# Kernel optimization log

Measured on AMD Instinct MI355X. Metric: run time of the kernel, lower is better.

Reference implementation:

```python
import jax, jax.numpy as jnp
import numpy as np

DIM = 512
NSLOTS = 8
ITERS = 3
EPS = 1e-8
LN_EPS = 1e-5
SCALE = DIM ** -0.5


def _ln(x, g, b):
    m = jnp.mean(x, axis=-1, keepdims=True)
    v = jnp.mean((x - m) ** 2, axis=-1, keepdims=True)
    return (x - m) / jnp.sqrt(v + LN_EPS) * g + b


def _gru(x, h, W_ih, W_hh, b_ih, b_hh):
    # PyTorch GRUCell, gate order r,z,n
    gi = x @ W_ih.T + b_ih
    gh = h @ W_hh.T + b_hh
    ir, iz, inn = jnp.split(gi, 3, axis=-1)
    hr, hz, hn = jnp.split(gh, 3, axis=-1)
    r = jax.nn.sigmoid(ir + hr)
    z = jax.nn.sigmoid(iz + hz)
    n = jnp.tanh(inn + r * hn)
    return (1.0 - z) * n + z * h


def _norm_attn(dots):
    # softmax over slot axis, then renormalize over token axis
    a = jax.nn.softmax(dots, axis=1)
    return a / (jnp.sum(a, axis=-1, keepdims=True) + EPS)


def setup_inputs() -> dict:
    key = jax.random.key(0)
    ks = jax.random.split(key, 16)
    b, na, ni = 32, 1024, 3136
    d, hd = DIM, DIM  # hidden_dim = max(dim, 128) = 512
    s = 0.02
    inp = {
        'inputs_audio': jax.random.normal(ks[0], (b, na, d), jnp.float32),
        'inputs_image': jax.random.normal(ks[1], (b, ni, d), jnp.float32),
        'slots_noise': jax.random.normal(ks[2], (b, NSLOTS, d), jnp.float32),
        'slots_mu': jax.random.normal(ks[3], (1, 1, d), jnp.float32),
        'slots_logsigma': jnp.zeros((1, 1, d), jnp.float32),
        'ln_in_g': jnp.ones((d,), jnp.float32), 'ln_in_b': jnp.zeros((d,), jnp.float32),
        'ln_slots_g': jnp.ones((d,), jnp.float32), 'ln_slots_b': jnp.zeros((d,), jnp.float32),
        'ln_ff_g': jnp.ones((d,), jnp.float32), 'ln_ff_b': jnp.zeros((d,), jnp.float32),
        'Wq': jax.random.normal(ks[4], (d, d), jnp.float32) * s, 'bq': jnp.zeros((d,), jnp.float32),
        'Wk': jax.random.normal(ks[5], (d, d), jnp.float32) * s, 'bk': jnp.zeros((d,), jnp.float32),
        'Wv': jax.random.normal(ks[6], (d, d), jnp.float32) * s, 'bv': jnp.zeros((d,), jnp.float32),
        'W_ih': jax.random.normal(ks[7], (3 * d, d), jnp.float32) * s,
        'W_hh': jax.random.normal(ks[8], (3 * d, d), jnp.float32) * s,
        'b_ih': jnp.zeros((3 * d,), jnp.float32), 'b_hh': jnp.zeros((3 * d,), jnp.float32),
        'W1': jax.random.normal(ks[9], (hd, d), jnp.float32) * s, 'b1': jnp.zeros((hd,), jnp.float32),
        'W2': jax.random.normal(ks[10], (d, hd), jnp.float32) * s, 'b2': jnp.zeros((d,), jnp.float32),
    }
    return inp


def reference(inputs_audio, inputs_image, slots_noise, slots_mu, slots_logsigma,
              ln_in_g, ln_in_b, ln_slots_g, ln_slots_b, ln_ff_g, ln_ff_b,
              Wq, bq, Wk, bk, Wv, bv, W_ih, W_hh, b_ih, b_hh, W1, b1, W2, b2):
    b, na, d = inputs_audio.shape
    slots0 = slots_mu + jnp.exp(slots_logsigma) * slots_noise  # [b, S, d]

    ia = _ln(inputs_audio, ln_in_g, ln_in_b)
    ii = _ln(inputs_image, ln_in_g, ln_in_b)
    k_a = ia @ Wk.T + bk
    v_a = ia @ Wv.T + bv
    k_i = ii @ Wk.T + bk
    v_i = ii @ Wv.T + bv

    def mlp(x):
        return jax.nn.relu(x @ W1.T + b1) @ W2.T + b2

    def step(slots, k, v):
        prev = slots
        sn = _ln(slots, ln_slots_g, ln_slots_b)
        q = sn @ Wq.T + bq
        dots = jnp.einsum('bid,bjd->bij', q, k) * SCALE
        attn = _norm_attn(dots)
        upd = jnp.einsum('bjd,bij->bid', v, attn)
        h = _gru(upd.reshape(-1, d), prev.reshape(-1, d), W_ih, W_hh, b_ih, b_hh)
        slots = h.reshape(b, -1, d)
        slots = slots + mlp(_ln(slots, ln_ff_g, ln_ff_b))
        return slots, q, attn

    slots_a, slots_i = slots0, slots0
    for _ in range(ITERS):
        slots_a, q_a, attn_a = step(slots_a, k_a, v_a)
        slots_i, q_i, attn_i = step(slots_i, k_i, v_i)

    cross_ai = _norm_attn(jnp.einsum('bid,bjd->bij', q_a, k_i) * SCALE)  # audio->image
    cross_ia = _norm_attn(jnp.einsum('bid,bjd->bij', q_i, k_a) * SCALE)  # image->audio

    return (slots_a, q_a, k_a, attn_a, cross_ia,
            slots_i, q_i, k_i, attn_i, cross_ai)
```

## Files before the change

kernel.cpp:

```cpp
#include <hip/hip_runtime.h>
#include <hip/hip_bf16.h>

#define DIM 512
#define EPS 1e-8f
#define LN_EPS 1e-5f
#define SCALE 0.04419417382415922f

typedef float f32x4 __attribute__((ext_vector_type(4)));
typedef __bf16 bf16;
typedef __bf16 bf16x8 __attribute__((ext_vector_type(8)));

typedef const __attribute__((address_space(1))) void gvoid;
typedef __attribute__((address_space(3))) void lvoid;

__device__ inline float bf2f_lo(unsigned u) { union { unsigned x; float f; } c; c.x = u << 16; return c.f; }
__device__ inline float bf2f_hi(unsigned u) { union { unsigned x; float f; } c; c.x = u & 0xffff0000u; return c.f; }

__global__ __launch_bounds__(256) void k_stats_convert(
    const float* __restrict__ x, bf16* __restrict__ xbf,
    float* __restrict__ stats, int M)
{
  int row = blockIdx.x * 4 + (threadIdx.x >> 6);
  int lane = threadIdx.x & 63;
  if (row >= M) return;
  const float* xr = x + (size_t)row * DIM;
  float4 a = *(const float4*)(xr + lane * 8);
  float4 b = *(const float4*)(xr + lane * 8 + 4);
  float s  = a.x + a.y + a.z + a.w + b.x + b.y + b.z + b.w;
  float ss = a.x*a.x + a.y*a.y + a.z*a.z + a.w*a.w
           + b.x*b.x + b.y*b.y + b.z*b.z + b.w*b.w;
  for (int off = 32; off; off >>= 1) { s += __shfl_xor(s, off); ss += __shfl_xor(ss, off); }
  float mean = s * (1.0f / DIM);
  float var  = ss * (1.0f / DIM) - mean * mean;
  float rs   = rsqrtf(var + LN_EPS);
  if (lane == 0) { stats[row * 2] = mean; stats[row * 2 + 1] = rs; }
  union { bf16 h[8]; uint4 u; } cv;
  cv.h[0] = (bf16)a.x; cv.h[1] = (bf16)a.y; cv.h[2] = (bf16)a.z; cv.h[3] = (bf16)a.w;
  cv.h[4] = (bf16)b.x; cv.h[5] = (bf16)b.y; cv.h[6] = (bf16)b.z; cv.h[7] = (bf16)b.w;
  *(uint4*)(xbf + (size_t)row * DIM + lane * 8) = cv.u;
}

__global__ __launch_bounds__(256) void k_stats512(
    const float* __restrict__ x, float* __restrict__ stats)
{
  int row = blockIdx.x * 4 + (threadIdx.x >> 6);
  int lane = threadIdx.x & 63;
  const float* xr = x + (size_t)row * DIM;
  float4 a = *(const float4*)(xr + lane * 8);
  float4 b = *(const float4*)(xr + lane * 8 + 4);
  float s  = a.x + a.y + a.z + a.w + b.x + b.y + b.z + b.w;
  float ss = a.x*a.x + a.y*a.y + a.z*a.z + a.w*a.w
           + b.x*b.x + b.y*b.y + b.z*b.z + b.w*b.w;
  for (int off = 32; off; off >>= 1) { s += __shfl_xor(s, off); ss += __shfl_xor(ss, off); }
  float mean = s * (1.0f / DIM);
  float rs   = rsqrtf(ss * (1.0f / DIM) - mean * mean + LN_EPS);
  if (lane == 0) { stats[row * 2] = mean; stats[row * 2 + 1] = rs; }
}

__global__ __launch_bounds__(64) void k_prep(
    const float* __restrict__ Wk, const float* __restrict__ bk,
    const float* __restrict__ Wv, const float* __restrict__ bv,
    const float* __restrict__ g_in, const float* __restrict__ b_in,
    const float* __restrict__ Wq, const float* __restrict__ bq,
    const float* __restrict__ g_s, const float* __restrict__ b_s,
    const float* __restrict__ W1, const float* __restrict__ b1,
    const float* __restrict__ g_f, const float* __restrict__ b_f,
    bf16* __restrict__ wbf, float* __restrict__ c12kv,
    float* __restrict__ Wqp, float* __restrict__ cq,
    float* __restrict__ W1p, float* __restrict__ c1f)
{
  int n = blockIdx.x; int lane = threadIdx.x;
  if (n < 1024) {
    const float* W = (n < DIM) ? (Wk + (size_t)n * DIM) : (Wv + (size_t)(n - DIM) * DIM);
    float bias = (n < DIM) ? bk[n] : bv[n - DIM];
    float s1 = 0.f, s2 = 0.f;
    union { bf16 h[8]; uint4 u; } cv;
#pragma unroll
    for (int j = 0; j < 8; ++j) {
      int d = lane * 8 + j;
      float w = W[d];
      float gw = g_in[d] * w;
      s1 += gw; s2 += b_in[d] * w;
      cv.h[j] = (bf16)gw;
    }
    *(uint4*)(wbf + (size_t)n * DIM + lane * 8) = cv.u;
    for (int off = 32; off; off >>= 1) { s1 += __shfl_xor(s1, off); s2 += __shfl_xor(s2, off); }
    if (lane == 0) { c12kv[n * 2] = s1; c12kv[n * 2 + 1] = s2 + bias; }
  } else {
    int m; const float* W; float bias; const float* g; const float* b;
    float* Wp; float* cc;
    if (n < 1536) { m = n - 1024; W = Wq + (size_t)m * DIM; bias = bq[m]; g = g_s; b = b_s; Wp = Wqp; cc = cq; }
    else          { m = n - 1536; W = W1 + (size_t)m * DIM; bias = b1[m]; g = g_f; b = b_f; Wp = W1p; cc = c1f; }
    float s1 = 0.f, s2 = 0.f;
    float arr[8];
#pragma unroll
    for (int j = 0; j < 8; ++j) {
      int d = lane * 8 + j;
      float w = W[d];
      float gw = g[d] * w;
      s1 += gw; s2 += b[d] * w;
      arr[j] = gw;
    }
    *(float4*)(Wp + (size_t)m * DIM + lane * 8)     = make_float4(arr[0], arr[1], arr[2], arr[3]);
    *(float4*)(Wp + (size_t)m * DIM + lane * 8 + 4) = make_float4(arr[4], arr[5], arr[6], arr[7]);
    for (int off = 32; off; off >>= 1) { s1 += __shfl_xor(s1, off); s2 += __shfl_xor(s2, off); }
    if (lane == 0) { cc[m * 2] = s1; cc[m * 2 + 1] = s2 + bias; }
  }
}

__global__ __launch_bounds__(256) void k_kv_gemm(
    const bf16* __restrict__ xbf, const bf16* __restrict__ wbf,
    const float* __restrict__ stats, const float* __restrict__ c12,
    float* __restrict__ kout, bf16* __restrict__ kbf, bf16* __restrict__ vbf,
    int nblk)
{
  __shared__ bf16 As[2][128 * 64];
  __shared__ bf16 Bs[2][128 * 64];
  const int t = threadIdx.x, wave = t >> 6, lane = t & 63;
  int bid = blockIdx.x;
  int rid = (bid & 7) * (nblk >> 3) + (bid >> 3);
  const int row0 = (rid >> 3) * 128, col0 = (rid & 7) * 128;
  f32x4 acc[4][4] = {};

  const int sr  = wave * 8 + (lane >> 3);
  const int sgl = ((lane & 7) ^ (lane >> 3)) * 8;
  const bf16* asrc = xbf + (size_t)(row0 + sr) * DIM + sgl;
  const bf16* bsrc = wbf + (size_t)(col0 + sr) * DIM + sgl;

  auto stage = [&](int buf, int k0) {
#pragma unroll
    for (int p = 0; p < 4; ++p) {
      __builtin_amdgcn_global_load_lds(
          (gvoid*)(asrc + (size_t)p * 32 * DIM + k0),
          (lvoid*)((char*)&As[buf][0] + (p * 256 + wave * 64) * 16), 16, 0, 0);
      __builtin_amdgcn_global_load_lds(
          (gvoid*)(bsrc + (size_t)p * 32 * DIM + k0),
          (lvoid*)((char*)&Bs[buf][0] + (p * 256 + wave * 64) * 16), 16, 0, 0);
    }
  };

  stage(0, 0);
  const int l15 = lane & 15, q16 = lane >> 4;
  const int wm = wave >> 1, wn = wave & 1;
  int cur = 0;
  for (int ks = 0; ks < 8; ++ks) {
    __syncthreads();
    if (ks < 7) stage(cur ^ 1, (ks + 1) * 64);
    const bf16* Ab = &As[cur][0];
    const bf16* Bb = &Bs[cur][0];
#pragma unroll
    for (int kk = 0; kk < 2; ++kk) {
      bf16x8 af[4], bfr[4];
#pragma unroll
      for (int mi = 0; mi < 4; ++mi) {
        int R = wm * 64 + mi * 16 + l15;
        int gp = (kk * 4 + q16) ^ (R & 7);
        af[mi] = *(const bf16x8*)(Ab + R * 64 + gp * 8);
      }
#pragma unroll
      for (int ni = 0; ni < 4; ++ni) {
        int R = wn * 64 + ni * 16 + l15;
        int gp = (kk * 4 + q16) ^ (R & 7);
        bfr[ni] = *(const bf16x8*)(Bb + R * 64 + gp * 8);
      }
#pragma unroll
      for (int mi = 0; mi < 4; ++mi)
#pragma unroll
        for (int ni = 0; ni < 4; ++ni)
          acc[mi][ni] = __builtin_amdgcn_mfma_f32_16x16x32_bf16(af[mi], bfr[ni], acc[mi][ni], 0, 0, 0);
    }
    cur ^= 1;
  }
  const int rbase = q16 * 4;
#pragma unroll
  for (int mi = 0; mi < 4; ++mi) {
#pragma unroll
    for (int reg = 0; reg < 4; ++reg) {
      int row = row0 + wm * 64 + mi * 16 + rbase + reg;
      float mean = stats[row * 2], rs = stats[row * 2 + 1];
#pragma unroll
      for (int ni = 0; ni < 4; ++ni) {
        int col = col0 + wn * 64 + ni * 16 + l15;
        float c1 = c12[col * 2], c2 = c12[col * 2 + 1];
        float outv = rs * acc[mi][ni][reg] - rs * mean * c1 + c2;
        if (col0 < DIM) {
          kout[(size_t)row * DIM + col] = outv;
          if (kbf) kbf[(size_t)row * DIM + col] = (bf16)outv;
        } else {
          vbf[(size_t)row * DIM + (col - DIM)] = (bf16)outv;
        }
      }
    }
  }
}

__global__ __launch_bounds__(256) void k_f2bf(
    const float* __restrict__ in, bf16* __restrict__ out)
{
  size_t i = ((size_t)blockIdx.x * 256 + threadIdx.x) * 8;
  float4 a = *(const float4*)(in + i);
  float4 b = *(const float4*)(in + i + 4);
  union { bf16 h[8]; uint4 u; } cv;
  cv.h[0] = (bf16)a.x; cv.h[1] = (bf16)a.y; cv.h[2] = (bf16)a.z; cv.h[3] = (bf16)a.w;
  cv.h[4] = (bf16)b.x; cv.h[5] = (bf16)b.y; cv.h[6] = (bf16)b.z; cv.h[7] = (bf16)b.w;
  *(uint4*)(out + i) = cv.u;
}

__global__ __launch_bounds__(256) void k_init_slots(
    const float* __restrict__ noise, const float* __restrict__ mu,
    const float* __restrict__ lsig, float* __restrict__ slots)
{
  int idx = blockIdx.x * 256 + threadIdx.x;
  int d = idx & (DIM - 1);
  float v = mu[d] + expf(lsig[d]) * noise[idx];
  slots[idx] = v;
  slots[131072 + idx] = v;
}

template <int MODE>
__global__ __launch_bounds__(128) void k_sgemm(
    const float* __restrict__ A, const float* __restrict__ B, int N,
    float* __restrict__ C,
    const float* __restrict__ c12, const float* __restrict__ stats,
    const float* __restrict__ bias, const float* __restrict__ invden,
    const float* __restrict__ R,
    float* __restrict__ outA, float* __restrict__ outI,
    bf16* __restrict__ qbf)
{
  __shared__ float As[32][33];
  __shared__ float Bs[64][33];
  int t = threadIdx.x;
  int m0 = blockIdx.y * 32, n0 = blockIdx.x * 64;
  float acc[4][4] = {};
  for (int k0 = 0; k0 < DIM; k0 += 32) {
    __syncthreads();
#pragma unroll
    for (int p = 0; p < 2; ++p) {
      int idx = p * 128 + t, r = idx >> 3, c4 = (idx & 7) * 4;
      float4 v = *(const float4*)(A + (size_t)(m0 + r) * DIM + k0 + c4);
      As[r][c4] = v.x; As[r][c4 + 1] = v.y; As[r][c4 + 2] = v.z; As[r][c4 + 3] = v.w;
    }
#pragma unroll
    for (int p = 0; p < 4; ++p) {
      int idx = p * 128 + t, r = idx >> 3, c4 = (idx & 7) * 4;
      float4 v = *(const float4*)(B + (size_t)(n0 + r) * DIM + k0 + c4);
      Bs[r][c4] = v.x; Bs[r][c4 + 1] = v.y; Bs[r][c4 + 2] = v.z; Bs[r][c4 + 3] = v.w;
    }
    __syncthreads();
    int tr = t >> 4, tc = t & 15;
#pragma unroll
    for (int k = 0; k < 32; ++k) {
      float a0 = As[tr * 4][k], a1 = As[tr * 4 + 1][k], a2 = As[tr * 4 + 2][k], a3 = As[tr * 4 + 3][k];
      float b0 = Bs[tc * 4][k], b1 = Bs[tc * 4 + 1][k], b2 = Bs[tc * 4 + 2][k], b3 = Bs[tc * 4 + 3][k];
      acc[0][0] += a0 * b0; acc[0][1] += a0 * b1; acc[0][2] += a0 * b2; acc[0][3] += a0 * b3;
      acc[1][0] += a1 * b0; acc[1][1] += a1 * b1; acc[1][2] += a1 * b2; acc[1][3] += a1 * b3;
      acc[2][0] += a2 * b0; acc[2][1] += a2 * b1; acc[2][2] += a2 * b2; acc[2][3] += a2 * b3;
      acc[3][0] += a3 * b0; acc[3][1] += a3 * b1; acc[3][2] += a3 * b2; acc[3][3] += a3 * b3;
    }
  }
  int tr = t >> 4, tc = t & 15;
#pragma unroll
  for (int mi = 0; mi < 4; ++mi) {
    int row = m0 + tr * 4 + mi;
#pragma unroll
    for (int ni = 0; ni < 4; ++ni) {
      int col = n0 + tc * 4 + ni;
      float v = acc[mi][ni];
      if (MODE == 0 || MODE == 3) {
        float mean = stats[row * 2], rs = stats[row * 2 + 1];
        v = rs * v - rs * mean * c12[col * 2] + c12[col * 2 + 1];
      }
      if (MODE == 1) v = v * invden[row] + bias[col];
      if (MODE == 2 || MODE == 4) v += bias[col];
      if (MODE == 3) v = fmaxf(v, 0.0f);
      if (MODE == 4) v += R[(size_t)row * N + col];
      if (MODE == 0) {
        if (row < 256) outA[(size_t)row * DIM + col] = v;
        else           outI[(size_t)(row - 256) * DIM + col] = v;
        qbf[(size_t)row * DIM + col] = (bf16)(v * SCALE);
      } else {
        C[(size_t)row * N + col] = v;
        if (MODE == 4 && outA) {
          if (row < 256) outA[(size_t)row * DIM + col] = v;
          else           outI[(size_t)(row - 256) * DIM + col] = v;
        }
      }
    }
  }
}

__global__ __launch_bounds__(256) void k_dots(
    const bf16* __restrict__ qA, const bf16* __restrict__ qI,
    const bf16* __restrict__ kA, const bf16* __restrict__ kI,
    float* __restrict__ aoutA, float* __restrict__ aoutI,
    float* __restrict__ denp, int NA_, int NI_)
{
  __shared__ bf16 ks[128 * 64];
  __shared__ float dsh[32];
  int t = threadIdx.x, wave = t >> 6, lane = t & 63;
  int b = blockIdx.y, tile = blockIdx.x;
  bool isA = tile < 8;
  int til = isA ? tile : tile - 8;
  int N = isA ? NA_ : NI_;
  int j0 = til * 128;
  const bf16* q = (isA ? qA : qI) + (size_t)b * 8 * DIM;
  const bf16* k = (isA ? kA : kI) + (size_t)b * N * DIM;
  float* aout = (isA ? aoutA : aoutI) + (size_t)b * 8 * N;
  int drow = (isA ? 0 : 256) + b * 8;

  const int l15 = lane & 15, q16 = lane >> 4;
  bf16x8 afq[16];
  {
    const bf16* qr = q + (size_t)(l15 & 7) * DIM + q16 * 8;
#pragma unroll
    for (int f = 0; f < 16; ++f)
      afq[f] = *(const bf16x8*)(qr + f * 32);
  }

  const int sr  = wave * 8 + (lane >> 3);
  const int sgl = ((lane & 7) ^ (lane >> 3)) * 8;
  f32x4 acc[2] = {};
  for (int c = 0; c < 8; ++c) {
    __syncthreads();
#pragma unroll
    for (int p = 0; p < 4; ++p) {
      int jr = j0 + p * 32 + sr;
      if (jr > N - 1) jr = N - 1;
      __builtin_amdgcn_global_load_lds(
          (gvoid*)(k + (size_t)jr * DIM + c * 64 + sgl),
          (lvoid*)((char*)ks + (p * 256 + wave * 64) * 16), 16, 0, 0);
    }
    __syncthreads();
#pragma unroll
    for (int kk = 0; kk < 2; ++kk) {
#pragma unroll
      for (int n = 0; n < 2; ++n) {
        int R = wave * 32 + n * 16 + l15;
        int gp = (kk * 4 + q16) ^ (R & 7);
        bf16x8 bfr = *(const bf16x8*)(ks + R * 64 + gp * 8);
        acc[n] = __builtin_amdgcn_mfma_f32_16x16x32_bf16(afq[c * 2 + kk], bfr, acc[n], 0, 0, 0);
      }
    }
  }

  float dsum[8];
#pragma unroll
  for (int i = 0; i < 8; ++i) dsum[i] = 0.f;
#pragma unroll
  for (int n = 0; n < 2; ++n) {
    int j = j0 + wave * 32 + n * 16 + l15;
    float dv[8];
#pragma unroll
    for (int r = 0; r < 4; ++r) {
      float own = acc[n][r];
      float oth = __shfl_xor(own, 16);
      if (q16 == 0) { dv[r] = own; dv[4 + r] = oth; }
      else          { dv[r] = oth; dv[4 + r] = own; }
    }
    float mx = dv[0];
#pragma unroll
    for (int i = 1; i < 8; ++i) mx = fmaxf(mx, dv[i]);
    float sum = 0.f;
#pragma unroll
    for (int i = 0; i < 8; ++i) { dv[i] = __expf(dv[i] - mx); sum += dv[i]; }
    float inv = 1.0f / sum;
    bool valid = (j < N);
#pragma unroll
    for (int i = 0; i < 8; ++i) {
      float av = valid ? dv[i] * inv : 0.0f;
      dsum[i] += av;
      if (valid && q16 == 0) aout[(size_t)i * N + j] = av;
    }
  }
#pragma unroll
  for (int i = 0; i < 8; ++i) {
    float v = dsum[i];
    v += __shfl_xor(v, 1); v += __shfl_xor(v, 2);
    v += __shfl_xor(v, 4); v += __shfl_xor(v, 8);
    dsum[i] = v;
  }
  if (lane == 0) {
#pragma unroll
    for (int i = 0; i < 8; ++i) dsh[wave * 8 + i] = dsum[i];
  }
  __syncthreads();
  if (t < 8) {
    float den = dsh[t] + dsh[8 + t] + dsh[16 + t] + dsh[24 + t];
    denp[((size_t)drow + t) * 32 + til] = den;
  }
}

__global__ __launch_bounds__(256) void k_upd(
    const bf16* __restrict__ vA, const bf16* __restrict__ vI,
    const float* __restrict__ aA, const float* __restrict__ aI,
    float* __restrict__ numpA, float* __restrict__ numpI, int NA_, int NI_)
{
  __shared__ float ash[128 * 12];
  int t = threadIdx.x, b = blockIdx.y, x = blockIdx.x;
  bool isA = x < 4;
  int c = isA ? x : x - 4;
  int N = isA ? NA_ : NI_;
  int nc = isA ? 4 : 13;
  int jstart = c * 256;
  int jend = jstart + 256; if (jend > N) jend = N;
  const bf16* v = (isA ? vA : vI) + (size_t)b * N * DIM;
  const float* a = (isA ? aA : aI) + (size_t)b * 8 * N;
  float acc[16] = {};
  int d0 = t * 2;
  for (int jt = jstart; jt < jend; jt += 128) {
    int jmax = jend - jt; if (jmax > 128) jmax = 128;
    __syncthreads();
    {
      int i = t >> 5, jq = (t & 31) * 4;
      float4 av = make_float4(0.f, 0.f, 0.f, 0.f);
      if (jt + jq < N) av = *(const float4*)&a[(size_t)i * N + jt + jq];
      ash[(jq + 0) * 12 + i] = av.x;
      ash[(jq + 1) * 12 + i] = av.y;
      ash[(jq + 2) * 12 + i] = av.z;
      ash[(jq + 3) * 12 + i] = av.w;
    }
    __syncthreads();
    for (int jj = 0; jj < jmax; ++jj) {
      unsigned vv = *(const unsigned*)(v + (size_t)(jt + jj) * DIM + d0);
      float v0 = bf2f_lo(vv), v1 = bf2f_hi(vv);
      float4 a0 = *(const float4*)&ash[jj * 12];
      float4 a1 = *(const float4*)&ash[jj * 12 + 4];
      acc[0]  += a0.x * v0; acc[1]  += a0.x * v1;
      acc[2]  += a0.y * v0; acc[3]  += a0.y * v1;
      acc[4]  += a0.z * v0; acc[5]  += a0.z * v1;
      acc[6]  += a0.w * v0; acc[7]  += a0.w * v1;
      acc[8]  += a1.x * v0; acc[9]  += a1.x * v1;
      acc[10] += a1.y * v0; acc[11] += a1.y * v1;
      acc[12] += a1.z * v0; acc[13] += a1.z * v1;
      acc[14] += a1.w * v0; acc[15] += a1.w * v1;
    }
  }
  float* np = (isA ? numpA : numpI) + (((size_t)b * nc + c) * 8) * DIM;
#pragma unroll
  for (int i = 0; i < 8; ++i)
    *(float2*)&np[(size_t)i * DIM + d0] = make_float2(acc[i * 2], acc[i * 2 + 1]);
}

__global__ __launch_bounds__(256) void k_numred(
    const float* __restrict__ numpA, const float* __restrict__ numpI,
    const float* __restrict__ denp,
    float* __restrict__ num, float* __restrict__ invden)
{
  int m = blockIdx.x, t = threadIdx.x;
  bool isA = m < 256;
  int mm = isA ? m : m - 256;
  int bb = mm >> 3, i = mm & 7;
  int nc = isA ? 4 : 13;
  const float* np = (isA ? numpA : numpI) + (((size_t)bb * nc) * 8 + i) * DIM;
  int d0 = t * 2;
  float s0 = 0.f, s1 = 0.f;
  for (int c = 0; c < nc; ++c) {
    float2 vv = *(const float2*)&np[(size_t)c * 8 * DIM + d0];
    s0 += vv.x; s1 += vv.y;
  }
  *(float2*)&num[(size_t)m * DIM + d0] = make_float2(s0, s1);
  if (t == 0) {
    int nch = isA ? 8 : 25;
    float den = EPS;
    for (int c2 = 0; c2 < nch; ++c2) den += denp[(size_t)m * 32 + c2];
    invden[m] = 1.0f / den;
  }
}

__global__ __launch_bounds__(256) void k_gru(
    const float* __restrict__ gi, const float* __restrict__ gh,
    const float* __restrict__ prev,
    float* __restrict__ hout, float* __restrict__ stats_h)
{
  int m = blockIdx.x; int t = threadIdx.x;
  size_t b3 = (size_t)m * 1536, b1 = (size_t)m * DIM;
  float h[2]; float s = 0.f, ss = 0.f;
#pragma unroll
  for (int p = 0; p < 2; ++p) {
    int d = t + p * 256;
    float ir = gi[b3 + d], iz = gi[b3 + 512 + d], in_ = gi[b3 + 1024 + d];
    float hr = gh[b3 + d], hz = gh[b3 + 512 + d], hn = gh[b3 + 1024 + d];
    float r = 1.f / (1.f + __expf(-(ir + hr)));
    float z = 1.f / (1.f + __expf(-(iz + hz)));
    float n = tanhf(in_ + r * hn);
    float hv = (1.f - z) * n + z * prev[b1 + d];
    hout[b1 + d] = hv;
    h[p] = hv; s += hv; ss += hv * hv;
  }
  for (int off = 32; off; off >>= 1) { s += __shfl_xor(s, off); ss += __shfl_xor(ss, off); }
  __shared__ float red[8];
  int wv = t >> 6, ln = t & 63;
  if (ln == 0) { red[wv] = s; red[4 + wv] = ss; }
  __syncthreads();
  s = red[0] + red[1] + red[2] + red[3];
  ss = red[4] + red[5] + red[6] + red[7];
  float mean = s * (1.0f / DIM);
  float rs = rsqrtf(ss * (1.0f / DIM) - mean * mean + LN_EPS);
  if (t == 0) { stats_h[m * 2] = mean; stats_h[m * 2 + 1] = rs; }
}

__global__ __launch_bounds__(256) void k_renorm2(
    const float* __restrict__ aA, const float* __restrict__ aI,
    const float* __restrict__ denp,
    float* __restrict__ outA, float* __restrict__ outI, int NA_, int NI_)
{
  int m = blockIdx.x; int t = threadIdx.x;
  bool isA = m < 256;
  int mm = isA ? m : m - 256;
  int N = isA ? NA_ : NI_;
  int nch = isA ? 8 : 25;
  const float* in = (isA ? aA : aI) + (size_t)mm * N;
  float* out = (isA ? outA : outI) + (size_t)mm * N;
  float den = EPS;
  for (int c = 0; c < nch; ++c) den += denp[(size_t)m * 32 + c];
  float inv = 1.0f / den;
  for (int idx = t; idx * 4 < N; idx += 256) {
    float4 v = *(const float4*)&in[idx * 4];
    v.x *= inv; v.y *= inv; v.z *= inv; v.w *= inv;
    *(float4*)&out[idx * 4] = v;
  }
}

extern "C" void kernel_launch(void* const* d_in, const int* in_sizes, int n_in,
                              void* d_out, int out_size, void* d_ws, size_t ws_size,
                              hipStream_t stream)
{
  (void)in_sizes; (void)n_in; (void)out_size;
  const float* x_a   = (const float*)d_in[0];
  const float* x_i   = (const float*)d_in[1];
  const float* noise = (const float*)d_in[2];
  const float* mu    = (const float*)d_in[3];
  const float* lsig  = (const float*)d_in[4];
  const float* ln_in_g = (const float*)d_in[5];
  const float* ln_in_b = (const float*)d_in[6];
  const float* ln_s_g  = (const float*)d_in[7];
  const float* ln_s_b  = (const float*)d_in[8];
  const float* ln_f_g  = (const float*)d_in[9];
  const float* ln_f_b  = (const float*)d_in[10];
  const float* Wq = (const float*)d_in[11]; const float* bq = (const float*)d_in[12];
  const float* Wk = (const float*)d_in[13]; const float* bk = (const float*)d_in[14];
  const float* Wv = (const float*)d_in[15]; const float* bv = (const float*)d_in[16];
  const float* W_ih = (const float*)d_in[17]; const float* W_hh = (const float*)d_in[18];
  const float* b_ih = (const float*)d_in[19]; const float* b_hh = (const float*)d_in[20];
  const float* W1 = (const float*)d_in[21]; const float* b1 = (const float*)d_in[22];
  const float* W2 = (const float*)d_in[23]; const float* b2 = (const float*)d_in[24];

  const int NA = 1024, NI = 3136;
  const int MA = 32 * NA, MI = 32 * NI;

  float* out = (float*)d_out;
  float* o_slots_a  = out;
  float* o_q_a      = out + 131072;
  float* o_k_a      = out + 262144;
  float* o_attn_a   = out + 17039360;
  float* o_cross_ia = out + 17301504;
  float* o_slots_i  = out + 17563648;
  float* o_q_i      = out + 17694720;
  float* o_k_i      = out + 17825792;
  float* o_attn_i   = out + 69206016;
  float* o_cross_ai = out + 70008832;

  char* w = (char*)d_ws;
  size_t used = 0;
  auto alloc = [&](size_t bytes) {
    char* p = w + used;
    used += (bytes + 255) & ~(size_t)255;
    return p;
  };
  bf16* xbf_a = (bf16*)alloc((size_t)MA * DIM * 2);
  bf16* xbf_i = (bf16*)alloc((size_t)MI * DIM * 2);
  bf16* vbf_a = (bf16*)alloc((size_t)MA * DIM * 2);
  bf16* vbf_i = (bf16*)alloc((size_t)MI * DIM * 2);
  float* stats_a = (float*)alloc((size_t)MA * 2 * 4);
  float* stats_i = (float*)alloc((size_t)MI * 2 * 4);
  bf16* wbf  = (bf16*)alloc(1024 * 512 * 2);
  float* c12kv = (float*)alloc(1024 * 2 * 4);
  float* Wqp = (float*)alloc(512 * 512 * 4);
  float* cq  = (float*)alloc(512 * 2 * 4);
  float* W1p = (float*)alloc(512 * 512 * 4);
  float* c1f = (float*)alloc(512 * 2 * 4);
  float* slots = (float*)alloc(512 * 512 * 4);
  bf16*  qbf   = (bf16*)alloc(512 * 512 * 2);
  float* mid   = (float*)alloc(512 * 512 * 4);
  float* hid   = (float*)alloc(512 * 512 * 4);
  float* num   = (float*)alloc(512 * 512 * 4);
  float* gib   = (float*)alloc(512 * 1536 * 4);
  float* ghb   = (float*)alloc(512 * 1536 * 4);
  float* stats_s = (float*)alloc(512 * 2 * 4);
  float* stats_h = (float*)alloc(512 * 2 * 4);
  float* invden  = (float*)alloc(512 * 4);
  float* denp    = (float*)alloc(512 * 32 * 4);
  float* abuf_a  = (float*)alloc((size_t)256 * NA * 4);
  float* abuf_i  = (float*)alloc((size_t)256 * NI * 4);
  float* numpA   = (float*)alloc((size_t)32 * 4 * 8 * DIM * 4);
  float* numpI   = (float*)alloc((size_t)32 * 13 * 8 * DIM * 4);
  if (used > ws_size) return;

  size_t kbf_bytes = (((size_t)MA * DIM * 2 + 255) & ~(size_t)255)
                   + (((size_t)MI * DIM * 2 + 255) & ~(size_t)255);
  bf16* kbf_a; bf16* kbf_i; bool kbf_fused;
  if (used + kbf_bytes <= ws_size) {
    kbf_a = (bf16*)alloc((size_t)MA * DIM * 2);
    kbf_i = (bf16*)alloc((size_t)MI * DIM * 2);
    kbf_fused = true;
  } else {
    kbf_a = xbf_a; kbf_i = xbf_i;
    kbf_fused = false;
  }

  k_stats_convert<<<MA / 4, 256, 0, stream>>>(x_a, xbf_a, stats_a, MA);
  k_stats_convert<<<MI / 4, 256, 0, stream>>>(x_i, xbf_i, stats_i, MI);
  k_prep<<<2048, 64, 0, stream>>>(Wk, bk, Wv, bv, ln_in_g, ln_in_b,
                                  Wq, bq, ln_s_g, ln_s_b, W1, b1, ln_f_g, ln_f_b,
                                  wbf, c12kv, Wqp, cq, W1p, c1f);
  k_kv_gemm<<<(MA / 128) * 8, 256, 0, stream>>>(xbf_a, wbf, stats_a, c12kv,
      o_k_a, kbf_fused ? kbf_a : nullptr, vbf_a, (MA / 128) * 8);
  k_kv_gemm<<<(MI / 128) * 8, 256, 0, stream>>>(xbf_i, wbf, stats_i, c12kv,
      o_k_i, kbf_fused ? kbf_i : nullptr, vbf_i, (MI / 128) * 8);
  if (!kbf_fused) {
    k_f2bf<<<MA * DIM / 2048, 256, 0, stream>>>(o_k_a, kbf_a);
    k_f2bf<<<MI * DIM / 2048, 256, 0, stream>>>(o_k_i, kbf_i);
  }
  k_init_slots<<<512, 256, 0, stream>>>(noise, mu, lsig, slots);
  k_stats512<<<128, 256, 0, stream>>>(slots, stats_s);

  for (int it = 0; it < 3; ++it) {
    bool last = (it == 2);
    k_sgemm<0><<<dim3(8, 16), 128, 0, stream>>>(slots, Wqp, DIM, nullptr,
        cq, stats_s, nullptr, nullptr, nullptr, o_q_a, o_q_i, qbf);
    k_dots<<<dim3(33, 32), 256, 0, stream>>>(qbf, qbf + 256 * DIM,
        kbf_a, kbf_i, abuf_a, abuf_i, denp, NA, NI);
    k_upd<<<dim3(17, 32), 256, 0, stream>>>(vbf_a, vbf_i, abuf_a, abuf_i, numpA, numpI, NA, NI);
    k_numred<<<512, 256, 0, stream>>>(numpA, numpI, denp, num, invden);
    k_sgemm<1><<<dim3(24, 16), 128, 0, stream>>>(num, W_ih, 1536, gib,
        nullptr, nullptr, b_ih, invden, nullptr, nullptr, nullptr, nullptr);
    k_sgemm<2><<<dim3(24, 16), 128, 0, stream>>>(slots, W_hh, 1536, ghb,
        nullptr, nullptr, b_hh, nullptr, nullptr, nullptr, nullptr, nullptr);
    k_gru<<<512, 256, 0, stream>>>(gib, ghb, slots, mid, stats_h);
    k_sgemm<3><<<dim3(8, 16), 128, 0, stream>>>(mid, W1p, DIM, hid,
        c1f, stats_h, nullptr, nullptr, nullptr, nullptr, nullptr, nullptr);
    k_sgemm<4><<<dim3(8, 16), 128, 0, stream>>>(hid, W2, DIM, slots,
        nullptr, nullptr, b2, nullptr, mid,
        last ? o_slots_a : nullptr, last ? o_slots_i : nullptr, nullptr);
    if (!last) k_stats512<<<128, 256, 0, stream>>>(slots, stats_s);
  }

  k_renorm2<<<512, 256, 0, stream>>>(abuf_a, abuf_i, denp, o_attn_a, o_attn_i, NA, NI);

  k_dots<<<dim3(33, 32), 256, 0, stream>>>(qbf + 256 * DIM, qbf,
      kbf_a, kbf_i, abuf_a, abuf_i, denp, NA, NI);
  k_renorm2<<<512, 256, 0, stream>>>(abuf_a, abuf_i, denp, o_cross_ia, o_cross_ai, NA, NI);
}
```

Baseline: 1.306 ms.

## Merge audio/image KV GEMMs into one launch with K=32 stages and vectorized epilogue

Combines the two K/V projection GEMM launches into a single grid that picks the audio or image operand per block. The K-step shrinks from 64 to 32, halving LDS use, and launch bounds request 4 blocks per CU to raise occupancy. MFMA operands are swapped so each lane holds four consecutive columns, letting the epilogue write float4 and packed bf16x4 stores. LN correction constants are split into separate c1/c2 arrays so they load as vectors. The cost is twice as many K-loop iterations and barriers per tile.

Measured after the change: 1.217 ms. 1.07x faster.

```diff
diff --git a/kernel.cpp b/kernel.cpp
--- a/kernel.cpp
+++ b/kernel.cpp
@@ -65,9 +65,9 @@
     const float* __restrict__ g_s, const float* __restrict__ b_s,
     const float* __restrict__ W1, const float* __restrict__ b1,
     const float* __restrict__ g_f, const float* __restrict__ b_f,
-    bf16* __restrict__ wbf, float* __restrict__ c12kv,
-    float* __restrict__ Wqp, float* __restrict__ cq,
-    float* __restrict__ W1p, float* __restrict__ c1f)
+    bf16* __restrict__ wbf, float* __restrict__ c1kv, float* __restrict__ c2kv,
+    float* __restrict__ Wqp, float* __restrict__ cq1, float* __restrict__ cq2,
+    float* __restrict__ W1p, float* __restrict__ cf1, float* __restrict__ cf2)
 {
   int n = blockIdx.x; int lane = threadIdx.x;
   if (n < 1024) {
@@ -85,12 +85,12 @@
     }
     *(uint4*)(wbf + (size_t)n * DIM + lane * 8) = cv.u;
     for (int off = 32; off; off >>= 1) { s1 += __shfl_xor(s1, off); s2 += __shfl_xor(s2, off); }
-    if (lane == 0) { c12kv[n * 2] = s1; c12kv[n * 2 + 1] = s2 + bias; }
+    if (lane == 0) { c1kv[n] = s1; c2kv[n] = s2 + bias; }
   } else {
     int m; const float* W; float bias; const float* g; const float* b;
-    float* Wp; float* cc;
-    if (n < 1536) { m = n - 1024; W = Wq + (size_t)m * DIM; bias = bq[m]; g = g_s; b = b_s; Wp = Wqp; cc = cq; }
-    else          { m = n - 1536; W = W1 + (size_t)m * DIM; bias = b1[m]; g = g_f; b = b_f; Wp = W1p; cc = c1f; }
+    float* Wp; float* cc1; float* cc2;
+    if (n < 1536) { m = n - 1024; W = Wq + (size_t)m * DIM; bias = bq[m]; g = g_s; b = b_s; Wp = Wqp; cc1 = cq1; cc2 = cq2; }
+    else          { m = n - 1536; W = W1 + (size_t)m * DIM; bias = b1[m]; g = g_f; b = b_f; Wp = W1p; cc1 = cf1; cc2 = cf2; }
     float s1 = 0.f, s2 = 0.f;
     float arr[8];
 #pragma unroll
@@ -104,91 +104,101 @@
     *(float4*)(Wp + (size_t)m * DIM + lane * 8)     = make_float4(arr[0], arr[1], arr[2], arr[3]);
     *(float4*)(Wp + (size_t)m * DIM + lane * 8 + 4) = make_float4(arr[4], arr[5], arr[6], arr[7]);
     for (int off = 32; off; off >>= 1) { s1 += __shfl_xor(s1, off); s2 += __shfl_xor(s2, off); }
-    if (lane == 0) { cc[m * 2] = s1; cc[m * 2 + 1] = s2 + bias; }
-  }
-}
-
-__global__ __launch_bounds__(256) void k_kv_gemm(
-    const bf16* __restrict__ xbf, const bf16* __restrict__ wbf,
-    const float* __restrict__ stats, const float* __restrict__ c12,
-    float* __restrict__ kout, bf16* __restrict__ kbf, bf16* __restrict__ vbf,
-    int nblk)
-{
-  __shared__ bf16 As[2][128 * 64];
-  __shared__ bf16 Bs[2][128 * 64];
+    if (lane == 0) { cc1[m] = s1; cc2[m] = s2 + bias; }
+  }
+}
+
+__global__ __launch_bounds__(256, 4) void k_kv_gemm(
+    const bf16* __restrict__ xa, const bf16* __restrict__ xi,
+    const bf16* __restrict__ wbf,
+    const float* __restrict__ sa, const float* __restrict__ si,
+    const float* __restrict__ c1, const float* __restrict__ c2,
+    float* __restrict__ ka, float* __restrict__ ki,
+    bf16* __restrict__ kba, bf16* __restrict__ kbi,
+    bf16* __restrict__ va, bf16* __restrict__ vi,
+    int nblkA, int nblkTot)
+{
+  __shared__ bf16 As[2][128 * 32];
+  __shared__ bf16 Bs[2][128 * 32];
   const int t = threadIdx.x, wave = t >> 6, lane = t & 63;
   int bid = blockIdx.x;
-  int rid = (bid & 7) * (nblk >> 3) + (bid >> 3);
-  const int row0 = (rid >> 3) * 128, col0 = (rid & 7) * 128;
+  int rid = (bid & 7) * (nblkTot >> 3) + (bid >> 3);
+  bool isA = rid < nblkA;
+  int lrid = isA ? rid : rid - nblkA;
+  const bf16* x = isA ? xa : xi;
+  const float* stats = isA ? sa : si;
+  float* kout = isA ? ka : ki;
+  bf16* kbf = isA ? kba : kbi;
+  bf16* vbf = isA ? va : vi;
+  const int row0 = (lrid >> 3) * 128, col0 = (lrid & 7) * 128;
   f32x4 acc[4][4] = {};
 
-  const int sr  = wave * 8 + (lane >> 3);
-  const int sgl = ((lane & 7) ^ (lane >> 3)) * 8;
-  const bf16* asrc = xbf + (size_t)(row0 + sr) * DIM + sgl;
+  const int sr  = wave * 16 + (lane >> 2);
+  const int sgl = ((lane & 3) ^ ((lane >> 3) & 3)) * 8;
+  const bf16* asrc = x   + (size_t)(row0 + sr) * DIM + sgl;
   const bf16* bsrc = wbf + (size_t)(col0 + sr) * DIM + sgl;
 
   auto stage = [&](int buf, int k0) {
 #pragma unroll
-    for (int p = 0; p < 4; ++p) {
+    for (int p = 0; p < 2; ++p) {
       __builtin_amdgcn_global_load_lds(
-          (gvoid*)(asrc + (size_t)p * 32 * DIM + k0),
+          (gvoid*)(asrc + (size_t)(p * 64) * DIM + k0),
           (lvoid*)((char*)&As[buf][0] + (p * 256 + wave * 64) * 16), 16, 0, 0);
       __builtin_amdgcn_global_load_lds(
-          (gvoid*)(bsrc + (size_t)p * 32 * DIM + k0),
+          (gvoid*)(bsrc + (size_t)(p * 64) * DIM + k0),
           (lvoid*)((char*)&Bs[buf][0] + (p * 256 + wave * 64) * 16), 16, 0, 0);
     }
   };
 
-  stage(0, 0);
   const int l15 = lane & 15, q16 = lane >> 4;
   const int wm = wave >> 1, wn = wave & 1;
+  const int gpx = (q16 ^ ((l15 >> 1) & 3)) * 8;
+
+  stage(0, 0);
   int cur = 0;
-  for (int ks = 0; ks < 8; ++ks) {
+  for (int ks = 0; ks < 16; ++ks) {
     __syncthreads();
-    if (ks < 7) stage(cur ^ 1, (ks + 1) * 64);
+    if (ks < 15) stage(cur ^ 1, (ks + 1) * 32);
     const bf16* Ab = &As[cur][0];
     const bf16* Bb = &Bs[cur][0];
-#pragma unroll
-    for (int kk = 0; kk < 2; ++kk) {
-      bf16x8 af[4], bfr[4];
-#pragma unroll
-      for (int mi = 0; mi < 4; ++mi) {
-        int R = wm * 64 + mi * 16 + l15;
-        int gp = (kk * 4 + q16) ^ (R & 7);
-        af[mi] = *(const bf16x8*)(Ab + R * 64 + gp * 8);
-      }
-#pragma unroll
-      for (int ni = 0; ni < 4; ++ni) {
-        int R = wn * 64 + ni * 16 + l15;
-        int gp = (kk * 4 + q16) ^ (R & 7);
-        bfr[ni] = *(const bf16x8*)(Bb + R * 64 + gp * 8);
-      }
+    bf16x8 ax[4], bw[4];
+#pragma unroll
+    for (int mi = 0; mi < 4; ++mi)
+      ax[mi] = *(const bf16x8*)(Ab + (wm * 64 + mi * 16 + l15) * 32 + gpx);
+#pragma unroll
+    for (int ni = 0; ni < 4; ++ni)
+      bw[ni] = *(const bf16x8*)(Bb + (wn * 64 + ni * 16 + l15) * 32 + gpx);
+#pragma unroll
+    for (int ni = 0; ni < 4; ++ni)
 #pragma unroll
       for (int mi = 0; mi < 4; ++mi)
-#pragma unroll
-        for (int ni = 0; ni < 4; ++ni)
-          acc[mi][ni] = __builtin_amdgcn_mfma_f32_16x16x32_bf16(af[mi], bfr[ni], acc[mi][ni], 0, 0, 0);
-    }
+        acc[ni][mi] = __builtin_amdgcn_mfma_f32_16x16x32_bf16(bw[ni], ax[mi], acc[ni][mi], 0, 0, 0);
     cur ^= 1;
   }
-  const int rbase = q16 * 4;
+
 #pragma unroll
   for (int mi = 0; mi < 4; ++mi) {
-#pragma unroll
-    for (int reg = 0; reg < 4; ++reg) {
-      int row = row0 + wm * 64 + mi * 16 + rbase + reg;
-      float mean = stats[row * 2], rs = stats[row * 2 + 1];
-#pragma unroll
-      for (int ni = 0; ni < 4; ++ni) {
-        int col = col0 + wn * 64 + ni * 16 + l15;
-        float c1 = c12[col * 2], c2 = c12[col * 2 + 1];
-        float outv = rs * acc[mi][ni][reg] - rs * mean * c1 + c2;
-        if (col0 < DIM) {
-          kout[(size_t)row * DIM + col] = outv;
-          if (kbf) kbf[(size_t)row * DIM + col] = (bf16)outv;
-        } else {
-          vbf[(size_t)row * DIM + (col - DIM)] = (bf16)outv;
-        }
+    int row = row0 + wm * 64 + mi * 16 + l15;
+    float2 st = *(const float2*)&stats[row * 2];
+    float rs = st.y, rm = st.y * st.x;
+#pragma unroll
+    for (int ni = 0; ni < 4; ++ni) {
+      int col = col0 + wn * 64 + ni * 16 + q16 * 4;
+      float4 c1v = *(const float4*)&c1[col];
+      float4 c2v = *(const float4*)&c2[col];
+      f32x4 a = acc[ni][mi];
+      float4 o;
+      o.x = rs * a[0] - rm * c1v.x + c2v.x;
+      o.y = rs * a[1] - rm * c1v.y + c2v.y;
+      o.z = rs * a[2] - rm * c1v.z + c2v.z;
+      o.w = rs * a[3] - rm * c1v.w + c2v.w;
+      union { bf16 h[4]; uint2 u; } pk;
+      pk.h[0] = (bf16)o.x; pk.h[1] = (bf16)o.y; pk.h[2] = (bf16)o.z; pk.h[3] = (bf16)o.w;
+      if (col0 < DIM) {
+        *(float4*)&kout[(size_t)row * DIM + col] = o;
+        if (kbf) *(uint2*)&kbf[(size_t)row * DIM + col] = pk.u;
+      } else {
+        *(uint2*)&vbf[(size_t)row * DIM + (col - DIM)] = pk.u;
       }
     }
   }
@@ -221,7 +231,8 @@
 __global__ __launch_bounds__(128) void k_sgemm(
     const float* __restrict__ A, const float* __restrict__ B, int N,
     float* __restrict__ C,
-    const float* __restrict__ c12, const float* __restrict__ stats,
+    const float* __restrict__ c1a, const float* __restrict__ c2a,
+    const float* __restrict__ stats,
     const float* __restrict__ bias, const float* __restrict__ invden,
     const float* __restrict__ R,
     float* __restrict__ outA, float* __restrict__ outI,
@@ -268,7 +279,7 @@
       float v = acc[mi][ni];
       if (MODE == 0 || MODE == 3) {
         float mean = stats[row * 2], rs = stats[row * 2 + 1];
-        v = rs * v - rs * mean * c12[col * 2] + c12[col * 2 + 1];
+        v = rs * v - rs * mean * c1a[col] + c2a[col];
       }
       if (MODE == 1) v = v * invden[row] + bias[col];
       if (MODE == 2 || MODE == 4) v += bias[col];
@@ -574,11 +585,14 @@
   float* stats_a = (float*)alloc((size_t)MA * 2 * 4);
   float* stats_i = (float*)alloc((size_t)MI * 2 * 4);
   bf16* wbf  = (bf16*)alloc(1024 * 512 * 2);
-  float* c12kv = (float*)alloc(1024 * 2 * 4);
+  float* c1kv = (float*)alloc(1024 * 4);
+  float* c2kv = (float*)alloc(1024 * 4);
   float* Wqp = (float*)alloc(512 * 512 * 4);
-  float* cq  = (float*)alloc(512 * 2 * 4);
+  float* cq1 = (float*)alloc(512 * 4);
+  float* cq2 = (float*)alloc(512 * 4);
   float* W1p = (float*)alloc(512 * 512 * 4);
-  float* c1f = (float*)alloc(512 * 2 * 4);
+  float* cf1 = (float*)alloc(512 * 4);
+  float* cf2 = (float*)alloc(512 * 4);
   float* slots = (float*)alloc(512 * 512 * 4);
   bf16*  qbf   = (bf16*)alloc(512 * 512 * 2);
   float* mid   = (float*)alloc(512 * 512 * 4);
@@ -612,11 +626,15 @@
   k_stats_convert<<<MI / 4, 256, 0, stream>>>(x_i, xbf_i, stats_i, MI);
   k_prep<<<2048, 64, 0, stream>>>(Wk, bk, Wv, bv, ln_in_g, ln_in_b,
                                   Wq, bq, ln_s_g, ln_s_b, W1, b1, ln_f_g, ln_f_b,
-                                  wbf, c12kv, Wqp, cq, W1p, c1f);
-  k_kv_gemm<<<(MA / 128) * 8, 256, 0, stream>>>(xbf_a, wbf, stats_a, c12kv,
-      o_k_a, kbf_fused ? kbf_a : nullptr, vbf_a, (MA / 128) * 8);
-  k_kv_gemm<<<(MI / 128) * 8, 256, 0, stream>>>(xbf_i, wbf, stats_i, c12kv,
-      o_k_i, kbf_fused ? kbf_i : nullptr, vbf_i, (MI / 128) * 8);
+                                  wbf, c1kv, c2kv, Wqp, cq1, cq2, W1p, cf1, cf2);
+  {
+    int nblkA = (MA / 128) * 8;
+    int nblkTot = nblkA + (MI / 128) * 8;
+    k_kv_gemm<<<nblkTot, 256, 0, stream>>>(xbf_a, xbf_i, wbf, stats_a, stats_i,
+        c1kv, c2kv, o_k_a, o_k_i,
+        kbf_fused ? kbf_a : nullptr, kbf_fused ? kbf_i : nullptr,
+        vbf_a, vbf_i, nblkA, nblkTot);
+  }
   if (!kbf_fused) {
     k_f2bf<<<MA * DIM / 2048, 256, 0, stream>>>(o_k_a, kbf_a);
     k_f2bf<<<MI * DIM / 2048, 256, 0, stream>>>(o_k_i, kbf_i);
@@ -627,20 +645,20 @@
   for (int it = 0; it < 3; ++it) {
     bool last = (it == 2);
     k_sgemm<0><<<dim3(8, 16), 128, 0, stream>>>(slots, Wqp, DIM, nullptr,
-        cq, stats_s, nullptr, nullptr, nullptr, o_q_a, o_q_i, qbf);
+        cq1, cq2, stats_s, nullptr, nullptr, nullptr, o_q_a, o_q_i, qbf);
     k_dots<<<dim3(33, 32), 256, 0, stream>>>(qbf, qbf + 256 * DIM,
         kbf_a, kbf_i, abuf_a, abuf_i, denp, NA, NI);
     k_upd<<<dim3(17, 32), 256, 0, stream>>>(vbf_a, vbf_i, abuf_a, abuf_i, numpA, numpI, NA, NI);
     k_numred<<<512, 256, 0, stream>>>(numpA, numpI, denp, num, invden);
     k_sgemm<1><<<dim3(24, 16), 128, 0, stream>>>(num, W_ih, 1536, gib,
-        nullptr, nullptr, b_ih, invden, nullptr, nullptr, nullptr, nullptr);
+        nullptr, nullptr, nullptr, b_ih, invden, nullptr, nullptr, nullptr, nullptr);
     k_sgemm<2><<<dim3(24, 16), 128, 0, stream>>>(slots, W_hh, 1536, ghb,
-        nullptr, nullptr, b_hh, nullptr, nullptr, nullptr, nullptr, nullptr);
+        nullptr, nullptr, nullptr, b_hh, nullptr, nullptr, nullptr, nullptr, nullptr);
     k_gru<<<512, 256, 0, stream>>>(gib, ghb, slots, mid, stats_h);
     k_sgemm<3><<<dim3(8, 16), 128, 0, stream>>>(mid, W1p, DIM, hid,
-        c1f, stats_h, nullptr, nullptr, nullptr, nullptr, nullptr, nullptr);
+        cf1, cf2, stats_h, nullptr, nullptr, nullptr, nullptr, nullptr, nullptr);
     k_sgemm<4><<<dim3(8, 16), 128, 0, stream>>>(hid, W2, DIM, slots,
-        nullptr, nullptr, b2, nullptr, mid,
+        nullptr, nullptr, nullptr, b2, nullptr, mid,
         last ? o_slots_a : nullptr, last ? o_slots_i : nullptr, nullptr);
     if (!last) k_stats512<<<128, 256, 0, stream>>>(slots, stats_s);
   }
```
